# Performance work log

Hardware: AMD Instinct MI355X
Metric: run time of the kernel (lower is better)

The kernel has to match this reference:

```python
import jax, jax.numpy as jnp
import numpy as np

V, H, B, T, L, G = 32000, 256, 16, 128, 50, 8
BETA, GAMMA = 5.0, 2.0
ATOL = 1e-8  # torch.allclose(x, zeros) default atol (rtol term vanishes vs zero)


def setup_inputs() -> dict:
    key = jax.random.key(0)
    ks = jax.random.split(key, 17)
    u = 1.0 / np.sqrt(H)
    def U(k, shape):
        return jax.random.uniform(k, shape, jnp.float32, -u, u)
    return dict(
        recipe=jax.random.randint(ks[0], (B, T), 0, V),
        g=jax.random.randint(ks[1], (B, G), 0, V),
        ingr=jax.random.randint(ks[2], (B, L), 0, V),
        wv=jax.random.normal(ks[3], (V, H), jnp.float32) * 0.1,  # frozen word vectors
        w_ih=U(ks[4], (5 * H, H)),
        w_hh=U(ks[5], (5 * H, H)),
        b_ih=U(ks[6], (5 * H,)),
        b_hh=U(ks[7], (5 * H,)),
        Z=U(ks[8], (H, H)),
        Y=U(ks[9], (H, H)),
        U_g=U(ks[10], (H, H)),
        z_bias=U(ks[11], (H,)),
        y_bias=U(ks[12], (H,)),
        S=U(ks[13], (3, H)),
        P=U(ks[14], (H, H)),
        fcW=U(ks[15], (V, H)),
        fcb=U(ks[16], (V,)),
    )


def _cgru_forward(x, g_vec, E, w_ih, w_hh, b_ih, b_hh, Z, Y, U_g, z_bias, y_bias, S, P):
    # x: (B,T,H) batch_first; g_vec: (B,H); E: (B,L,H)
    ht0 = g_vec @ U_g.T                      # init_hidden
    a0 = jnp.zeros((x.shape[0], E.shape[1]), x.dtype)
    E0 = E                                   # (1-a)*E with a=0
    ot0 = jnp.zeros_like(x[:, 0])
    goal_term = g_vec @ Y.T + y_bias         # constant across steps

    def step(carry, x_t):
        ht, ot, a, E_new = carry
        is_zero = jnp.all(jnp.abs(x_t) <= ATOL)
        # --- cell ---
        gi = x_t @ w_ih.T + b_ih
        gh = ht @ w_hh.T + b_hh
        i_r, i_u, i_n, i_g, i_i = jnp.split(gi, 5, axis=1)
        h_r, h_u, h_n, h_g, h_i = jnp.split(gh, 5, axis=1)
        z_t = jax.nn.sigmoid(i_u + h_u)
        r_t = jax.nn.sigmoid(i_r + h_r)
        s_t = jax.nn.sigmoid(i_g + h_g)
        q_t = jax.nn.sigmoid(i_i + h_i)
        tmp = E_new.sum(axis=1)              # 'mlk -> mk'
        h_tilde = jnp.tanh(i_n + r_t * h_n + s_t * goal_term + q_t * (tmp @ Z.T + z_bias))
        ht2 = h_tilde + z_t * (ht - h_tilde)
        # --- attention read/write ---
        ref = jax.nn.softmax((BETA * ht2) @ S.T, axis=-1)   # (B,3)
        h_proj = ht2 @ P.T
        En = (1.0 - a)[:, :, None] * E
        alpha_n = jax.nn.softmax(GAMMA * jnp.einsum('mk,mlk->ml', h_proj, En), axis=-1)
        c_n = jnp.einsum('mlk,ml->mk', E, alpha_n)
        Eu = a[:, :, None] * E
        alpha_u = jax.nn.softmax(GAMMA * jnp.einsum('mk,mlk->ml', h_proj, Eu), axis=-1)
        c_u = jnp.einsum('mlk,ml->mk', E, alpha_u)
        out = ref[:, 0:1] * h_proj + ref[:, 1:2] * c_n + ref[:, 2:3] * c_u
        a2 = a + ref[:, 1:2] * alpha_n
        # skip update when input step is all-zero (faithful to torch.allclose guard)
        ht_o = jnp.where(is_zero, ht, ht2)
        ot_o = jnp.where(is_zero, ot, out)
        a_o = jnp.where(is_zero, a, a2)
        E_o = jnp.where(is_zero, E_new, En)
        return (ht_o, ot_o, a_o, E_o), ot_o

    (ht, ot, a, E_new), outs = jax.lax.scan(step, (ht0, ot0, a0, E0),
                                            jnp.transpose(x, (1, 0, 2)))
    output = jnp.transpose(outs, (1, 0, 2))  # back to batch_first (B,T,H)
    return output, ht, a, E_new


def reference(recipe, g, ingr, wv, w_ih, w_hh, b_ih, b_hh, Z, Y, U_g,
              z_bias, y_bias, S, P, fcW, fcb):
    recipe_embed = wv[recipe]           # (B,T,H)
    goal_embed = wv[g].sum(axis=1)      # (B,H)
    E = wv[ingr]                        # (B,L,H)
    output, ht, a, E_new = _cgru_forward(recipe_embed, goal_embed, E,
                                         w_ih, w_hh, b_ih, b_hh, Z, Y, U_g,
                                         z_bias, y_bias, S, P)
    logits = output @ fcW.T + fcb       # (B,T,V)
    return logits, ht, a, E_new
```

## Files before the change

### kernel.cpp

```cpp
#include <hip/hip_runtime.h>

#define Hd   256
#define Bd   16
#define Td   128
#define Ld   50
#define Vd   32000
#define G5H  1280

typedef __attribute__((ext_vector_type(8))) short short8v;
typedef __attribute__((ext_vector_type(4))) float f32x4;

__device__ __forceinline__ unsigned short f2bu(float f) {
  unsigned u = __float_as_uint(f);
  unsigned r = (u + 0x7fffu + ((u >> 16) & 1u)) >> 16;
  return (unsigned short)r;
}
__device__ __forceinline__ float bu2f(unsigned short b) {
  return __uint_as_float(((unsigned)b) << 16);
}
__device__ __forceinline__ float sigm(float x) { return 1.f / (1.f + __expf(-x)); }

__device__ __forceinline__ void st_devu(unsigned* p, unsigned v) {
  __hip_atomic_store(p, v, __ATOMIC_RELAXED, __HIP_MEMORY_SCOPE_AGENT);
}
__device__ __forceinline__ unsigned ld_devu(const unsigned* p) {
  return __hip_atomic_load((unsigned*)p, __ATOMIC_RELAXED, __HIP_MEMORY_SCOPE_AGENT);
}
__device__ __forceinline__ void st_devd(double* p, double v) {
  __hip_atomic_store(p, v, __ATOMIC_RELAXED, __HIP_MEMORY_SCOPE_AGENT);
}
__device__ __forceinline__ double ld_devd(const double* p) {
  return __hip_atomic_load((double*)p, __ATOMIC_RELAXED, __HIP_MEMORY_SCOPE_AGENT);
}
__device__ __forceinline__ double pk2(float a, float b) {
  union { double d; float2 f; } u; u.f = make_float2(a, b); return u.d;
}

__global__ __launch_bounds__(256) void conv_kernel(
    const float* __restrict__ wv, const float* __restrict__ w_ih,
    const float* __restrict__ fcW, const float* __restrict__ w_hh,
    const float* __restrict__ Zm, const float* __restrict__ Pm,
    unsigned short* __restrict__ wv_b, unsigned short* __restrict__ wih_b,
    unsigned short* __restrict__ fcw_b, unsigned short* __restrict__ whh_f,
    unsigned short* __restrict__ z_f, unsigned short* __restrict__ p_f)
{
  const long N0 = 2048000, N1 = N0 + 81920, N2 = N1 + 2048000;
  const long NW = 81920, NZ = 16384, NP = 16384;
  const long N5 = N2 + NW + NZ + NP;
  for (long idx = (long)blockIdx.x * blockDim.x + threadIdx.x; idx < N5;
       idx += (long)gridDim.x * blockDim.x) {
    if (idx < N2) {
      const float* src; unsigned short* dst; long off;
      if      (idx < N0) { src = wv;   dst = wv_b;  off = idx; }
      else if (idx < N1) { src = w_ih; dst = wih_b; off = idx - N0; }
      else               { src = fcW;  dst = fcw_b; off = idx - N1; }
      float4 v = *(const float4*)(src + off * 4);
      ushort4 o;
      o.x = f2bu(v.x); o.y = f2bu(v.y); o.z = f2bu(v.z); o.w = f2bu(v.w);
      *(ushort4*)(dst + off * 4) = o;
    } else {
      long u = idx - N2;
      const float* src; unsigned short* dst;
      if      (u < NW)      { src = w_hh; dst = whh_f; }
      else if (u < NW + NZ) { src = Zm;   dst = z_f;  u -= NW; }
      else                  { src = Pm;   dst = p_f;  u -= NW + NZ; }
      long frag = u >> 7;
      int g128 = (int)(u & 127);
      int lane = g128 >> 1, e0 = (g128 & 1) * 4;
      long T = frag >> 3; int ks = (int)(frag & 7);
      int lr = lane & 15, lg = lane >> 4;
      float4 v = *(const float4*)(src + (T * 16 + lr) * 256 + ks * 32 + lg * 8 + e0);
      ushort4 o;
      o.x = f2bu(v.x); o.y = f2bu(v.y); o.z = f2bu(v.z); o.w = f2bu(v.w);
      *(ushort4*)(dst + u * 4) = o;
    }
  }
}

__global__ __launch_bounds__(256) void prep_kernel(
    const int* __restrict__ g, const int* __restrict__ ingr,
    const float* __restrict__ wv, const float* __restrict__ Ug,
    const float* __restrict__ Ym, const float* __restrict__ yb,
    float* __restrict__ E_ws, float* __restrict__ sumE,
    float* __restrict__ goal_ws, float* __restrict__ HT0)
{
  __shared__ float ge[256];
  const int b = blockIdx.x, tid = threadIdx.x;
  float s = 0.f;
  for (int i = 0; i < 8; ++i) s += wv[((size_t)g[(b << 3) + i] << 8) + tid];
  ge[tid] = s;
  __syncthreads();
  float h0 = 0.f, gt = 0.f;
  const float* ur = Ug + (tid << 8);
  const float* yr = Ym + (tid << 8);
#pragma unroll 8
  for (int k = 0; k < Hd; k += 4) {
    float4 gv = *(const float4*)(ge + k);
    float4 uv = *(const float4*)(ur + k);
    float4 yv = *(const float4*)(yr + k);
    h0 = fmaf(gv.x, uv.x, h0); h0 = fmaf(gv.y, uv.y, h0);
    h0 = fmaf(gv.z, uv.z, h0); h0 = fmaf(gv.w, uv.w, h0);
    gt = fmaf(gv.x, yv.x, gt); gt = fmaf(gv.y, yv.y, gt);
    gt = fmaf(gv.z, yv.z, gt); gt = fmaf(gv.w, yv.w, gt);
  }
  HT0[(b << 8) + tid] = h0;
  goal_ws[(b << 8) + tid] = gt + yb[tid];
  float se = 0.f;
  for (int l = 0; l < Ld; ++l) {
    float v = wv[((size_t)ingr[b * Ld + l] << 8) + tid];
    E_ws[((size_t)(b * Ld + l) << 8) + tid] = v;
    se += v;
  }
  sumE[(b << 8) + tid] = se;
}

template <int MODE>
__global__ __launch_bounds__(256) void gemm_bf16(
    const unsigned short* __restrict__ A, const unsigned short* __restrict__ Bmat,
    const int* __restrict__ ridx, const float* __restrict__ bias,
    float* __restrict__ C)
{
  __shared__ unsigned short As[128 * 64];
  __shared__ unsigned short Bs[128 * 64];
  const int tid = threadIdx.x;
  const int m0 = blockIdx.x << 7, n0 = blockIdx.y << 7;
  const int wave = tid >> 6, lane = tid & 63;
  const int wm = wave >> 1, wn = wave & 1;
  const int lr = lane & 15, lg = lane >> 4;

  f32x4 acc[4][4];
#pragma unroll
  for (int i = 0; i < 4; ++i)
#pragma unroll
    for (int jj = 0; jj < 4; ++jj) acc[i][jj] = (f32x4){0.f, 0.f, 0.f, 0.f};

  const int srow = tid >> 1, shalf = tid & 1;
  const unsigned short* arow;
  {
    int gm = m0 + srow;
    if (MODE == 0) {
      int tt = gm >> 4, bb = gm & 15;
      arow = A + (size_t)ridx[bb * Td + tt] * Hd;
    } else {
      arow = A + (size_t)gm * Hd;
    }
  }
  const unsigned short* brow = Bmat + (size_t)(n0 + srow) * Hd;

  for (int k0 = 0; k0 < Hd; k0 += 64) {
#pragma unroll
    for (int c = 0; c < 4; ++c) {
      int k = shalf * 32 + c * 8;
      uint4 va = *(const uint4*)(arow + k0 + k);
      uint4 vb = *(const uint4*)(brow + k0 + k);
      int byo = (srow << 7) + ((k << 1) ^ ((srow & 7) << 4));
      *(uint4*)((char*)As + byo) = va;
      *(uint4*)((char*)Bs + byo) = vb;
    }
    __syncthreads();
#pragma unroll
    for (int kk = 0; kk < 2; ++kk) {
      short8v af[4], bfr[4];
      const int kb = kk * 32 + lg * 8;
#pragma unroll
      for (int i = 0; i < 4; ++i) {
        int ar = wm * 64 + i * 16 + lr;
        af[i] = *(const short8v*)((const char*)As + (ar << 7) + ((kb << 1) ^ ((ar & 7) << 4)));
        int br = wn * 64 + i * 16 + lr;
        bfr[i] = *(const short8v*)((const char*)Bs + (br << 7) + ((kb << 1) ^ ((br & 7) << 4)));
      }
#pragma unroll
      for (int i = 0; i < 4; ++i)
#pragma unroll
        for (int jj = 0; jj < 4; ++jj)
          acc[i][jj] = __builtin_amdgcn_mfma_f32_16x16x32_bf16(af[i], bfr[jj], acc[i][jj], 0, 0, 0);
    }
    __syncthreads();
  }
#pragma unroll
  for (int i = 0; i < 4; ++i)
#pragma unroll
    for (int jj = 0; jj < 4; ++jj) {
      int col = n0 + wn * 64 + jj * 16 + lr;
      float bv = bias[col];
#pragma unroll
      for (int r = 0; r < 4; ++r) {
        int row = m0 + wm * 64 + i * 16 + lg * 4 + r;
        float v = acc[i][jj][r] + bv;
        if (MODE == 0) {
          int tt = row >> 4, bb = row & 15;
          C[((size_t)(bb * Td + tt)) * G5H + col] = v;
        } else {
          C[(size_t)row * Vd + col] = v;
        }
      }
    }
}

#define RNN_SMEM 150080
__global__ __launch_bounds__(512, 1) void rnn_kernel(
    const unsigned short* __restrict__ whh_f, const unsigned short* __restrict__ z_f,
    const unsigned short* __restrict__ p_f, const float* __restrict__ b_hh,
    const float* __restrict__ Sm, const float* __restrict__ z_bias,
    const float* __restrict__ gi, const float* __restrict__ goal_ws,
    const float* __restrict__ E_ws, const float* __restrict__ sumE,
    const float* __restrict__ HT0,
    unsigned short* __restrict__ out_all, float* __restrict__ d_out,
    double* __restrict__ XH, double* __restrict__ XP, unsigned* __restrict__ FL)
{
  extern __shared__ char smem[];
  unsigned short* w_lds = (unsigned short*)(smem);
  unsigned short* z_lds = (unsigned short*)(smem + 81920);
  unsigned short* p_lds = (unsigned short*)(smem + 98304);
  unsigned short* E_lds = (unsigned short*)(smem + 114688);
  float* hp    = (float*)(smem + 141088);
  float* gh_l  = (float*)(smem + 142112);
  float* zd    = (float*)(smem + 142752);
  float* se    = (float*)(smem + 142880);
  float* gl    = (float*)(smem + 143904);
  float* bh    = (float*)(smem + 144032);
  float* zb    = (float*)(smem + 144672);
  float* Sl    = (float*)(smem + 144800);
  float* a_l   = (float*)(smem + 145184);
  float* d_l   = (float*)(smem + 145440);
  float* an_l  = (float*)(smem + 145696);
  float* au_l  = (float*)(smem + 145952);
  float* sd    = (float*)(smem + 146208);
  float* refl  = (float*)(smem + 146224);
  unsigned short* tp_hi = (unsigned short*)(smem + 146240);
  unsigned short* tp_lo = (unsigned short*)(smem + 146752);
  unsigned short* hs_hi = (unsigned short*)(smem + 147264);
  unsigned short* hs_lo = (unsigned short*)(smem + 147328);
  float* hrow  = (float*)(smem + 147392);
  unsigned short* ht_hi = (unsigned short*)(smem + 148416);
  unsigned short* ht_lo = (unsigned short*)(smem + 148928);
  float* gi_l  = (float*)(smem + 149440);

  const int b  = blockIdx.x >> 3;
  const int j  = blockIdx.x & 7;
  const int hc0 = j << 5;
  const int tid = threadIdx.x;
  const int lane = tid & 63, wid = tid >> 6;
  const int lr = lane & 15, lg = lane >> 4;
  unsigned* FLb = FL + (b << 5);

  for (int idx = tid; idx < 5120; idx += 512) {
    int f = idx >> 6, e = idx & 63;
    int q = f >> 3, ks = f & 7;
    int T = (q >> 1) * 16 + 2 * j + (q & 1);
    *(uint4*)(w_lds + ((size_t)f << 9) + e * 8) =
        *(const uint4*)(whh_f + (((size_t)T * 8 + ks) << 9) + e * 8);
  }
  for (int idx = tid; idx < 1024; idx += 512) {
    int f = idx >> 6, e = idx & 63;
    int T = 2 * j + (f >> 3), ks = f & 7;
    *(uint4*)(z_lds + ((size_t)f << 9) + e * 8) =
        *(const uint4*)(z_f + (((size_t)T * 8 + ks) << 9) + e * 8);
  }
  for (int idx = tid; idx < 1024; idx += 512) {
    int f = idx >> 6, e = idx & 63;
    *(uint4*)(p_lds + ((size_t)f << 9) + e * 8) =
        *(const uint4*)(p_f + (((size_t)f * 8 + j) << 9) + e * 8);
  }
  for (int idx = tid; idx < Ld * 256; idx += 512) {
    int l = idx >> 8, k = idx & 255;
    E_lds[l * 264 + (k >> 5) * 33 + (k & 31)] =
        f2bu(E_ws[((size_t)(b * Ld + l) << 8) + k]);
  }
  if (tid < 160) bh[tid] = b_hh[((tid >> 5) << 8) + hc0 + (tid & 31)];
  if (tid < 96) Sl[tid] = Sm[((tid >> 5) << 8) + hc0 + (tid & 31)];
  if (tid < 32) {
    gl[tid] = goal_ws[(b << 8) + hc0 + tid];
    zb[tid] = z_bias[hc0 + tid];
  }
  if (tid < 256) {
    float s0 = sumE[(b << 8) + tid];
    se[tid] = s0;
    unsigned short hi = f2bu(s0);
    tp_hi[tid] = hi; tp_lo[tid] = f2bu(s0 - bu2f(hi));
    float h0 = HT0[(b << 8) + tid];
    hrow[tid] = h0;
    unsigned short hh = f2bu(h0);
    ht_hi[tid] = hh; ht_lo[tid] = f2bu(h0 - bu2f(hh));
  }
  if (tid < 64) a_l[tid] = 0.f;
  __syncthreads();

  if (wid < 4) {
#pragma unroll
    for (int i = 0; i < 3; ++i) {
      int q = wid + 4 * i;
      if (q < 10) {
        f32x4 acc = (f32x4){0.f, 0.f, 0.f, 0.f};
#pragma unroll
        for (int ks = 0; ks < 8; ++ks) {
          short8v av = *(const short8v*)(w_lds + ((size_t)(q * 8 + ks) << 9) + (lane << 3));
          short8v bv = (short8v){0,0,0,0,0,0,0,0};
          if (lr < 2)
            bv = *(const short8v*)((lr == 0 ? ht_hi : ht_lo) + ks * 32 + (lg << 3));
          acc = __builtin_amdgcn_mfma_f32_16x16x32_bf16(av, bv, acc, 0, 0, 0);
        }
#pragma unroll
        for (int r = 0; r < 4; ++r) {
          float v = acc[r] + __shfl_xor(acc[r], 1);
          if (lr == 0) gh_l[q * 16 + lg * 4 + r] = v;
        }
      }
    }
  } else if (wid == 4 || wid == 5) {
    int tz = wid - 4;
    f32x4 acc = (f32x4){0.f, 0.f, 0.f, 0.f};
#pragma unroll
    for (int ks = 0; ks < 8; ++ks) {
      short8v av = *(const short8v*)(z_lds + ((size_t)(tz * 8 + ks) << 9) + (lane << 3));
      short8v bv = (short8v){0,0,0,0,0,0,0,0};
      if (lr < 2)
        bv = *(const short8v*)((lr == 0 ? tp_hi : tp_lo) + ks * 32 + (lg << 3));
      acc = __builtin_amdgcn_mfma_f32_16x16x32_bf16(av, bv, acc, 0, 0, 0);
    }
#pragma unroll
    for (int r = 0; r < 4; ++r) {
      float v = acc[r] + __shfl_xor(acc[r], 1);
      if (lr == 0) zd[tz * 16 + lg * 4 + r] = v;
    }
  }
  __syncthreads();
  {
    double* XHp = XH + ((size_t)((0 * 16 + b) * 8 + j)) * 16;
    double* XPp = XP + ((size_t)((0 * 16 + b) * 8 + j)) * 132;
    if (tid < 32) {
      int cl = tid;
      const float* gib = gi + ((size_t)(b * Td)) * G5H + hc0 + cl;
      float g_ir = gib[0], g_iu = gib[256], g_in = gib[512];
      float g_ig = gib[768], g_ii = gib[1024];
      float hr = gh_l[cl]       + bh[cl];
      float hu = gh_l[32 + cl]  + bh[32 + cl];
      float hn = gh_l[64 + cl]  + bh[64 + cl];
      float hg = gh_l[96 + cl]  + bh[96 + cl];
      float hq = gh_l[128 + cl] + bh[128 + cl];
      float rt = sigm(g_ir + hr), zt = sigm(g_iu + hu);
      float st = sigm(g_ig + hg), qt = sigm(g_ii + hq);
      float htl = tanhf(g_in + rt * hn + st * gl[cl] + qt * (zd[cl] + zb[cl]));
      float h2 = htl + zt * (hrow[hc0 + cl] - htl);
      unsigned short hi = f2bu(h2);
      hs_hi[cl] = hi; hs_lo[cl] = f2bu(h2 - bu2f(hi));
      float h2o = __shfl_xor(h2, 1);
      if (!(cl & 1)) st_devd(XHp + (cl >> 1), pk2(h2, h2o));
      float p0 = Sl[cl] * h2, p1 = Sl[32 + cl] * h2, p2 = Sl[64 + cl] * h2;
      p0 += __shfl_xor(p0, 1);  p0 += __shfl_xor(p0, 2);  p0 += __shfl_xor(p0, 4);
      p0 += __shfl_xor(p0, 8);  p0 += __shfl_xor(p0, 16);
      p1 += __shfl_xor(p1, 1);  p1 += __shfl_xor(p1, 2);  p1 += __shfl_xor(p1, 4);
      p1 += __shfl_xor(p1, 8);  p1 += __shfl_xor(p1, 16);
      p2 += __shfl_xor(p2, 1);  p2 += __shfl_xor(p2, 2);  p2 += __shfl_xor(p2, 4);
      p2 += __shfl_xor(p2, 8);  p2 += __shfl_xor(p2, 16);
      if (cl == 0) {
        st_devd(XPp + 128, pk2(p0, p1));
        st_devd(XPp + 129, pk2(p2, 0.f));
      }
    }
    __syncthreads();
#pragma unroll
    for (int qq = 0; qq < 2; ++qq) {
      int q = wid * 2 + qq;
      short8v av = *(const short8v*)(p_lds + ((size_t)q << 9) + (lane << 3));
      short8v bv = (short8v){0,0,0,0,0,0,0,0};
      if (lr < 2)
        bv = *(const short8v*)((lr == 0 ? hs_hi : hs_lo) + (lg << 3));
      f32x4 acc = (f32x4){0.f, 0.f, 0.f, 0.f};
      acc = __builtin_amdgcn_mfma_f32_16x16x32_bf16(av, bv, acc, 0, 0, 0);
      float v0 = acc[0] + __shfl_xor(acc[0], 1);
      float v1 = acc[1] + __shfl_xor(acc[1], 1);
      float v2 = acc[2] + __shfl_xor(acc[2], 1);
      float v3 = acc[3] + __shfl_xor(acc[3], 1);
      if (lr == 0) {
        st_devd(XPp + q * 8 + lg * 2, pk2(v0, v1));
        st_devd(XPp + q * 8 + lg * 2 + 1, pk2(v2, v3));
      }
    }
    asm volatile("s_waitcnt vmcnt(0)" ::: "memory");
    __syncthreads();
    if (tid == 0) st_devu(FLb + j, 1u);
  }

  for (int t = 0; t < Td; ++t) {
    const int par = t & 1, par1 = (t + 1) & 1;
    const double* XPr = XP + ((size_t)((par * 16 + b) * 8)) * 132;
    const double* XHr = XH + ((size_t)((par * 16 + b) * 8)) * 16;
    double* XPp = XP + ((size_t)((par1 * 16 + b) * 8 + j)) * 132;
    double* XHp = XH + ((size_t)((par1 * 16 + b) * 8 + j)) * 16;
    if (tid < 64) {
      unsigned tgt = (unsigned)(t + 1);
      int guard = 0;
      while (1) {
        unsigned v = (lane < 8) ? ld_devu(FLb + lane) : tgt;
        if (__all((int)(v >= tgt))) break;
        __builtin_amdgcn_s_sleep(1);
        if (++guard > (1 << 20)) break;
      }
    }
    __syncthreads();
    if (tid < 128) {
      float2 f0, f1, f2, f3, f4, f5, f6, f7;
      { union { double d; float2 f; } u_;
        u_.d = ld_devd(XPr + 0 * 132 + tid); f0 = u_.f;
        u_.d = ld_devd(XPr + 1 * 132 + tid); f1 = u_.f;
        u_.d = ld_devd(XPr + 2 * 132 + tid); f2 = u_.f;
        u_.d = ld_devd(XPr + 3 * 132 + tid); f3 = u_.f;
        u_.d = ld_devd(XPr + 4 * 132 + tid); f4 = u_.f;
        u_.d = ld_devd(XPr + 5 * 132 + tid); f5 = u_.f;
        u_.d = ld_devd(XPr + 6 * 132 + tid); f6 = u_.f;
        u_.d = ld_devd(XPr + 7 * 132 + tid); f7 = u_.f; }
      hp[2 * tid] =
        ((((((f0.x + f1.x) + f2.x) + f3.x) + f4.x) + f5.x) + f6.x) + f7.x;
      hp[2 * tid + 1] =
        ((((((f0.y + f1.y) + f2.y) + f3.y) + f4.y) + f5.y) + f6.y) + f7.y;
    } else if (tid == 128 || tid == 129) {
      int w = tid - 128;
      float2 f[8];
#pragma unroll
      for (int js = 0; js < 8; ++js) {
        union { double d; float2 f; } u_;
        u_.d = ld_devd(XPr + js * 132 + 128 + w);
        f[js] = u_.f;
      }
      float sx = ((((((f[0].x + f[1].x) + f[2].x) + f[3].x) + f[4].x) + f[5].x)
                  + f[6].x) + f[7].x;
      float sy = ((((((f[0].y + f[1].y) + f[2].y) + f[3].y) + f[4].y) + f[5].y)
                  + f[6].y) + f[7].y;
      if (w == 0) { sd[0] = sx; sd[1] = sy; }
      else        { sd[2] = sx; }
    } else if (tid >= 256 && tid < 384) {
      int u = tid - 256;
      union { double d; float2 f; } u_;
      u_.d = ld_devd(XHr + (u >> 4) * 16 + (u & 15));
      int c0 = (u >> 4) * 32 + 2 * (u & 15);
      float a0 = u_.f.x, a1 = u_.f.y;
      hrow[c0] = a0; hrow[c0 + 1] = a1;
      unsigned short h0 = f2bu(a0), h1 = f2bu(a1);
      ht_hi[c0] = h0;     ht_lo[c0] = f2bu(a0 - bu2f(h0));
      ht_hi[c0 + 1] = h1; ht_lo[c0 + 1] = f2bu(a1 - bu2f(h1));
      if (t == Td - 1 && j == 0) {
        d_out[(size_t)65536000 + (b << 8) + c0] = a0;
        d_out[(size_t)65536000 + (b << 8) + c0 + 1] = a1;
      }
    } else if (tid >= 384 && tid < 416 && t < Td - 1) {
      int u2 = tid - 384;
      const float* gib = gi + ((size_t)(b * Td + t + 1)) * G5H + hc0 + u2;
      gi_l[u2]       = gib[0];
      gi_l[32 + u2]  = gib[256];
      gi_l[64 + u2]  = gib[512];
      gi_l[96 + u2]  = gib[768];
      gi_l[128 + u2] = gib[1024];
    }
    __syncthreads();
    if (wid < 4) {
#pragma unroll
      for (int i = 0; i < 3; ++i) {
        int q = wid + 4 * i;
        if (q < 10) {
          f32x4 acc = (f32x4){0.f, 0.f, 0.f, 0.f};
#pragma unroll
          for (int ks = 0; ks < 8; ++ks) {
            short8v av = *(const short8v*)(w_lds + ((size_t)(q * 8 + ks) << 9) + (lane << 3));
            short8v bv = (short8v){0,0,0,0,0,0,0,0};
            if (lr < 2)
              bv = *(const short8v*)((lr == 0 ? ht_hi : ht_lo) + ks * 32 + (lg << 3));
            acc = __builtin_amdgcn_mfma_f32_16x16x32_bf16(av, bv, acc, 0, 0, 0);
          }
#pragma unroll
          for (int r = 0; r < 4; ++r) {
            float v = acc[r] + __shfl_xor(acc[r], 1);
            if (lr == 0) gh_l[q * 16 + lg * 4 + r] = v;
          }
        }
      }
    } else if (tid >= 256) {
      int u = tid - 256;
      if (u < 200) {
        int l = u >> 2, q = u & 3;
        const unsigned short* er0 = E_lds + l * 264 + q * 66;
        const float* hq = hp + (q << 6);
        float p = 0.f;
#pragma unroll 8
        for (int i = 0; i < 16; ++i) {
          unsigned uu = *(const unsigned*)(er0 + 2 * i);
          float e0 = __uint_as_float(uu << 16);
          float e1 = __uint_as_float(uu & 0xffff0000u);
          p = fmaf(e0, hq[2 * i], p);
          p = fmaf(e1, hq[2 * i + 1], p);
        }
        const unsigned short* er1 = er0 + 33;
        const float* hq1 = hq + 32;
#pragma unroll 8
        for (int i = 0; i < 16; ++i) {
          unsigned uu = *(const unsigned*)(er1 + 2 * i);
          float e0 = __uint_as_float(uu << 16);
          float e1 = __uint_as_float(uu & 0xffff0000u);
          p = fmaf(e0, hq1[2 * i], p);
          p = fmaf(e1, hq1[2 * i + 1], p);
        }
        p += __shfl_xor(p, 1); p += __shfl_xor(p, 2);
        if (q == 0) d_l[l] = p;
      } else if (u == 224) {
        float s0 = 5.0f * sd[0], s1 = 5.0f * sd[1], s2 = 5.0f * sd[2];
        float m = fmaxf(s0, fmaxf(s1, s2));
        float e0 = __expf(s0 - m), e1 = __expf(s1 - m), e2 = __expf(s2 - m);
        float inv = 1.f / (e0 + e1 + e2);
        refl[0] = e0 * inv; refl[1] = e1 * inv; refl[2] = e2 * inv;
      }
    }
    __syncthreads();
    if (tid >= 256 && tid < 384) {
      int u = tid - 256;
      int which = u >> 6;
      int l = u & 63;
      float dv;
      if (which == 0) dv = (l < Ld) ? 2.0f * (1.f - a_l[l]) * d_l[l] : -3.4e38f;
      else            dv = (l < Ld) ? 2.0f * a_l[l] * d_l[l]         : -3.4e38f;
      float m = dv;
      m = fmaxf(m, __shfl_xor(m, 1));  m = fmaxf(m, __shfl_xor(m, 2));
      m = fmaxf(m, __shfl_xor(m, 4));  m = fmaxf(m, __shfl_xor(m, 8));
      m = fmaxf(m, __shfl_xor(m, 16)); m = fmaxf(m, __shfl_xor(m, 32));
      float e = (l < Ld) ? __expf(dv - m) : 0.f;
      float ss = e;
      ss += __shfl_xor(ss, 1);  ss += __shfl_xor(ss, 2);  ss += __shfl_xor(ss, 4);
      ss += __shfl_xor(ss, 8);  ss += __shfl_xor(ss, 16); ss += __shfl_xor(ss, 32);
      float al = e / ss;
      if (which == 0) an_l[l] = al; else au_l[l] = al;
    }
    __syncthreads();
    if (tid >= 256) {
      int k = tid - 256;
      int kp = (k >> 5) * 33 + (k & 31);
      float accn = 0.f, accu = 0.f, acct = 0.f;
#pragma unroll 10
      for (int l = 0; l < Ld; ++l) {
        float e = bu2f(E_lds[l * 264 + kp]);
        accn = fmaf(an_l[l], e, accn);
        accu = fmaf(au_l[l], e, accu);
        acct = fmaf(a_l[l], e, acct);
      }
      float outv = refl[0] * hp[k] + refl[1] * accn + refl[2] * accu;
      float tn = se[k] - acct;
      unsigned short th = f2bu(tn);
      tp_hi[k] = th; tp_lo[k] = f2bu(tn - bu2f(th));
      if ((t & 7) == j) {
        out_all[(((b << 7) + t) << 8) + k] = f2bu(outv);
        if (t == Td - 1) {
          for (int l = 0; l < Ld; ++l) {
            size_t o = ((size_t)(b * Ld + l) << 8) + k;
            d_out[(size_t)65540896 + o] = (1.f - a_l[l]) * E_ws[o];
          }
        }
      }
    }
    __syncthreads();
    if (tid < 128) {
      int tz = wid;
      f32x4 acc = (f32x4){0.f, 0.f, 0.f, 0.f};
#pragma unroll
      for (int ks = 0; ks < 8; ++ks) {
        short8v av = *(const short8v*)(z_lds + ((size_t)(tz * 8 + ks) << 9) + (lane << 3));
        short8v bv = (short8v){0,0,0,0,0,0,0,0};
        if (lr < 2)
          bv = *(const short8v*)((lr == 0 ? tp_hi : tp_lo) + ks * 32 + (lg << 3));
        acc = __builtin_amdgcn_mfma_f32_16x16x32_bf16(av, bv, acc, 0, 0, 0);
      }
#pragma unroll
      for (int r = 0; r < 4; ++r) {
        float v = acc[r] + __shfl_xor(acc[r], 1);
        if (lr == 0) zd[tz * 16 + lg * 4 + r] = v;
      }
    } else if (tid >= 256 && tid < 256 + Ld) {
      int l = tid - 256;
      float na = a_l[l] + refl[1] * an_l[l];
      a_l[l] = na;
      if (t == Td - 1 && j == 7) d_out[(size_t)65540096 + b * Ld + l] = na;
    }
    __syncthreads();
    if (t < Td - 1 && tid < 32) {
      int cl = tid;
      float hr = gh_l[cl]       + bh[cl];
      float hu = gh_l[32 + cl]  + bh[32 + cl];
      float hn = gh_l[64 + cl]  + bh[64 + cl];
      float hg = gh_l[96 + cl]  + bh[96 + cl];
      float hq = gh_l[128 + cl] + bh[128 + cl];
      float rt = sigm(gi_l[cl] + hr), zt = sigm(gi_l[32 + cl] + hu);
      float st = sigm(gi_l[96 + cl] + hg), qt = sigm(gi_l[128 + cl] + hq);
      float htl = tanhf(gi_l[64 + cl] + rt * hn + st * gl[cl] + qt * (zd[cl] + zb[cl]));
      float h2 = htl + zt * (hrow[hc0 + cl] - htl);
      unsigned short hi = f2bu(h2);
      hs_hi[cl] = hi; hs_lo[cl] = f2bu(h2 - bu2f(hi));
      float h2o = __shfl_xor(h2, 1);
      if (!(cl & 1)) st_devd(XHp + (cl >> 1), pk2(h2, h2o));
      float p0 = Sl[cl] * h2, p1 = Sl[32 + cl] * h2, p2 = Sl[64 + cl] * h2;
      p0 += __shfl_xor(p0, 1);  p0 += __shfl_xor(p0, 2);  p0 += __shfl_xor(p0, 4);
      p0 += __shfl_xor(p0, 8);  p0 += __shfl_xor(p0, 16);
      p1 += __shfl_xor(p1, 1);  p1 += __shfl_xor(p1, 2);  p1 += __shfl_xor(p1, 4);
      p1 += __shfl_xor(p1, 8);  p1 += __shfl_xor(p1, 16);
      p2 += __shfl_xor(p2, 1);  p2 += __shfl_xor(p2, 2);  p2 += __shfl_xor(p2, 4);
      p2 += __shfl_xor(p2, 8);  p2 += __shfl_xor(p2, 16);
      if (cl == 0) {
        st_devd(XPp + 128, pk2(p0, p1));
        st_devd(XPp + 129, pk2(p2, 0.f));
      }
    }
    __syncthreads();
    if (t < Td - 1) {
#pragma unroll
      for (int qq = 0; qq < 2; ++qq) {
        int q = wid * 2 + qq;
        short8v av = *(const short8v*)(p_lds + ((size_t)q << 9) + (lane << 3));
        short8v bv = (short8v){0,0,0,0,0,0,0,0};
        if (lr < 2)
          bv = *(const short8v*)((lr == 0 ? hs_hi : hs_lo) + (lg << 3));
        f32x4 acc = (f32x4){0.f, 0.f, 0.f, 0.f};
        acc = __builtin_amdgcn_mfma_f32_16x16x32_bf16(av, bv, acc, 0, 0, 0);
        float v0 = acc[0] + __shfl_xor(acc[0], 1);
        float v1 = acc[1] + __shfl_xor(acc[1], 1);
        float v2 = acc[2] + __shfl_xor(acc[2], 1);
        float v3 = acc[3] + __shfl_xor(acc[3], 1);
        if (lr == 0) {
          st_devd(XPp + q * 8 + lg * 2, pk2(v0, v1));
          st_devd(XPp + q * 8 + lg * 2 + 1, pk2(v2, v3));
        }
      }
    }
    asm volatile("s_waitcnt vmcnt(0)" ::: "memory");
    __syncthreads();
    if (t < Td - 1 && tid == 0) st_devu(FLb + j, (unsigned)(t + 2));
  }
}

extern "C" void kernel_launch(void* const* d_in, const int* in_sizes, int n_in,
                              void* d_out, int out_size, void* d_ws, size_t ws_size,
                              hipStream_t stream)
{
  const int*   recipe = (const int*)d_in[0];
  const int*   g      = (const int*)d_in[1];
  const int*   ingr   = (const int*)d_in[2];
  const float* wv     = (const float*)d_in[3];
  const float* w_ih   = (const float*)d_in[4];
  const float* w_hh   = (const float*)d_in[5];
  const float* b_ih   = (const float*)d_in[6];
  const float* b_hh   = (const float*)d_in[7];
  const float* Z      = (const float*)d_in[8];
  const float* Y      = (const float*)d_in[9];
  const float* Ug     = (const float*)d_in[10];
  const float* z_bias = (const float*)d_in[11];
  const float* y_bias = (const float*)d_in[12];
  const float* S      = (const float*)d_in[13];
  const float* P      = (const float*)d_in[14];
  const float* fcW    = (const float*)d_in[15];
  const float* fcb    = (const float*)d_in[16];
  float* out = (float*)d_out;
  char* ws = (char*)d_ws;

  size_t off = 0;
  unsigned* FL             = (unsigned*)(ws + off);        off += 2048;
  double* XH               = (double*)(ws + off);          off += 32768;
  double* XP               = (double*)(ws + off);          off += 270336;
  unsigned short* wv_b     = (unsigned short*)(ws + off);  off += 16384000;
  unsigned short* wih_b    = (unsigned short*)(ws + off);  off += 655360;
  unsigned short* fcw_b    = (unsigned short*)(ws + off);  off += 16384000;
  unsigned short* whh_f    = (unsigned short*)(ws + off);  off += 655360;
  unsigned short* z_f      = (unsigned short*)(ws + off);  off += 131072;
  unsigned short* p_f      = (unsigned short*)(ws + off);  off += 131072;
  float* gi_ws             = (float*)(ws + off);           off += 10485760;
  float* E_ws              = (float*)(ws + off);           off += 819200;
  float* sumE              = (float*)(ws + off);           off += 16384;
  float* goal_ws           = (float*)(ws + off);           off += 16384;
  float* HT0               = (float*)(ws + off);           off += 16384;
  unsigned short* out_all  = (unsigned short*)(ws + off);  off += 1048576;

  hipMemsetAsync(FL, 0, 2048, stream);
  conv_kernel<<<4096, 256, 0, stream>>>(wv, w_ih, fcW, w_hh, Z, P,
                                        wv_b, wih_b, fcw_b, whh_f, z_f, p_f);
  prep_kernel<<<16, 256, 0, stream>>>(g, ingr, wv, Ug, Y, y_bias,
                                      E_ws, sumE, goal_ws, HT0);
  gemm_bf16<0><<<dim3(16, 10), 256, 0, stream>>>(wv_b, wih_b, recipe, b_ih, gi_ws);
  hipFuncSetAttribute((const void*)rnn_kernel,
                      hipFuncAttributeMaxDynamicSharedMemorySize, RNN_SMEM);
  rnn_kernel<<<128, 512, RNN_SMEM, stream>>>(whh_f, z_f, p_f, b_hh, S, z_bias,
                                             gi_ws, goal_ws, E_ws, sumE, HT0,
                                             out_all, out, XH, XP, FL);
  gemm_bf16<1><<<dim3(16, 250), 256, 0, stream>>>(out_all, fcw_b, nullptr, fcb, out);
}
```

Measured before the change: 1.530 ms.

## Reschedule recurrent step to overlap off-critical work with inter-block wait

Reorders the per-timestep phases of the persistent recurrent kernel. Computing the a-weighted E sum for the Z-projection input moves into the first phase, where it runs alongside the spin-wait on other blocks' flags. The Z matmul now runs in parallel with the w_hh matmul, and the GRU cell update runs alongside the attention softmax. This removes about two block barriers per step and shortens the critical path between publishing partial results and the next step. The cost is more complex warp-role assignment and ordering hazards around a_l, whose update is moved after the output computation.

After: 1.405 ms. 8.2% less time.

```diff
diff --git a/kernel.cpp b/kernel.cpp
--- a/kernel.cpp
+++ b/kernel.cpp
@@ -388,7 +388,17 @@
     const double* XHr = XH + ((size_t)((par * 16 + b) * 8)) * 16;
     double* XPp = XP + ((size_t)((par1 * 16 + b) * 8 + j)) * 132;
     double* XHp = XH + ((size_t)((par1 * 16 + b) * 8 + j)) * 16;
-    if (tid < 64) {
+    if (tid < 256) {
+      int k = tid;
+      int kp = (k >> 5) * 33 + (k & 31);
+      float acct = 0.f;
+#pragma unroll 10
+      for (int l = 0; l < Ld; ++l)
+        acct = fmaf(a_l[l], bu2f(E_lds[l * 264 + kp]), acct);
+      float tn = se[k] - acct;
+      unsigned short th = f2bu(tn);
+      tp_hi[k] = th; tp_lo[k] = f2bu(tn - bu2f(th));
+    } else {
       unsigned tgt = (unsigned)(t + 1);
       int guard = 0;
       while (1) {
@@ -397,84 +407,106 @@
         __builtin_amdgcn_s_sleep(1);
         if (++guard > (1 << 20)) break;
       }
+      int u = tid - 256;
+      if (u < 128) {
+        float2 f0, f1, f2, f3, f4, f5, f6, f7;
+        { union { double d; float2 f; } u_;
+          u_.d = ld_devd(XPr + 0 * 132 + u); f0 = u_.f;
+          u_.d = ld_devd(XPr + 1 * 132 + u); f1 = u_.f;
+          u_.d = ld_devd(XPr + 2 * 132 + u); f2 = u_.f;
+          u_.d = ld_devd(XPr + 3 * 132 + u); f3 = u_.f;
+          u_.d = ld_devd(XPr + 4 * 132 + u); f4 = u_.f;
+          u_.d = ld_devd(XPr + 5 * 132 + u); f5 = u_.f;
+          u_.d = ld_devd(XPr + 6 * 132 + u); f6 = u_.f;
+          u_.d = ld_devd(XPr + 7 * 132 + u); f7 = u_.f; }
+        hp[2 * u] =
+          ((((((f0.x + f1.x) + f2.x) + f3.x) + f4.x) + f5.x) + f6.x) + f7.x;
+        hp[2 * u + 1] =
+          ((((((f0.y + f1.y) + f2.y) + f3.y) + f4.y) + f5.y) + f6.y) + f7.y;
+      } else if (u < 192) {
+        int d0 = 2 * (u - 128);
+#pragma unroll
+        for (int s = 0; s < 2; ++s) {
+          int d = d0 + s;
+          union { double d; float2 f; } u_;
+          u_.d = ld_devd(XHr + (d >> 4) * 16 + (d & 15));
+          int c0 = (d >> 4) * 32 + 2 * (d & 15);
+          float a0 = u_.f.x, a1 = u_.f.y;
+          hrow[c0] = a0; hrow[c0 + 1] = a1;
+          unsigned short h0 = f2bu(a0), h1 = f2bu(a1);
+          ht_hi[c0] = h0;     ht_lo[c0] = f2bu(a0 - bu2f(h0));
+          ht_hi[c0 + 1] = h1; ht_lo[c0 + 1] = f2bu(a1 - bu2f(h1));
+          if (t == Td - 1 && j == 0) {
+            d_out[(size_t)65536000 + (b << 8) + c0] = a0;
+            d_out[(size_t)65536000 + (b << 8) + c0 + 1] = a1;
+          }
+        }
+      } else {
+        int u2 = u - 192;
+        if (u2 < 3) {
+          float2 f[8];
+#pragma unroll
+          for (int js = 0; js < 8; ++js) {
+            union { double d; float2 f; } u_;
+            u_.d = ld_devd(XPr + js * 132 + 128 + (u2 >> 1));
+            f[js] = u_.f;
+          }
+          float sx, sy;
+          sx = ((((((f[0].x + f[1].x) + f[2].x) + f[3].x) + f[4].x) + f[5].x)
+                + f[6].x) + f[7].x;
+          sy = ((((((f[0].y + f[1].y) + f[2].y) + f[3].y) + f[4].y) + f[5].y)
+                + f[6].y) + f[7].y;
+          sd[u2] = (u2 & 1) ? sy : ((u2 == 0) ? sx : sx);
+          if (u2 == 0) { sd[0] = sx; sd[1] = sy; }
+          else if (u2 == 2) sd[2] = sx;
+        } else if (u2 >= 8 && u2 < 40 && t < Td - 1) {
+          int c = u2 - 8;
+          const float* gib = gi + ((size_t)(b * Td + t + 1)) * G5H + hc0 + c;
+          gi_l[c]       = gib[0];
+          gi_l[32 + c]  = gib[256];
+          gi_l[64 + c]  = gib[512];
+          gi_l[96 + c]  = gib[768];
+          gi_l[128 + c] = gib[1024];
+        }
+      }
     }
     __syncthreads();
-    if (tid < 128) {
-      float2 f0, f1, f2, f3, f4, f5, f6, f7;
-      { union { double d; float2 f; } u_;
-        u_.d = ld_devd(XPr + 0 * 132 + tid); f0 = u_.f;
-        u_.d = ld_devd(XPr + 1 * 132 + tid); f1 = u_.f;
-        u_.d = ld_devd(XPr + 2 * 132 + tid); f2 = u_.f;
-        u_.d = ld_devd(XPr + 3 * 132 + tid); f3 = u_.f;
-        u_.d = ld_devd(XPr + 4 * 132 + tid); f4 = u_.f;
-        u_.d = ld_devd(XPr + 5 * 132 + tid); f5 = u_.f;
-        u_.d = ld_devd(XPr + 6 * 132 + tid); f6 = u_.f;
-        u_.d = ld_devd(XPr + 7 * 132 + tid); f7 = u_.f; }
-      hp[2 * tid] =
-        ((((((f0.x + f1.x) + f2.x) + f3.x) + f4.x) + f5.x) + f6.x) + f7.x;
-      hp[2 * tid + 1] =
-        ((((((f0.y + f1.y) + f2.y) + f3.y) + f4.y) + f5.y) + f6.y) + f7.y;
-    } else if (tid == 128 || tid == 129) {
-      int w = tid - 128;
-      float2 f[8];
-#pragma unroll
-      for (int js = 0; js < 8; ++js) {
-        union { double d; float2 f; } u_;
-        u_.d = ld_devd(XPr + js * 132 + 128 + w);
-        f[js] = u_.f;
-      }
-      float sx = ((((((f[0].x + f[1].x) + f[2].x) + f[3].x) + f[4].x) + f[5].x)
-                  + f[6].x) + f[7].x;
-      float sy = ((((((f[0].y + f[1].y) + f[2].y) + f[3].y) + f[4].y) + f[5].y)
-                  + f[6].y) + f[7].y;
-      if (w == 0) { sd[0] = sx; sd[1] = sy; }
-      else        { sd[2] = sx; }
-    } else if (tid >= 256 && tid < 384) {
-      int u = tid - 256;
-      union { double d; float2 f; } u_;
-      u_.d = ld_devd(XHr + (u >> 4) * 16 + (u & 15));
-      int c0 = (u >> 4) * 32 + 2 * (u & 15);
-      float a0 = u_.f.x, a1 = u_.f.y;
-      hrow[c0] = a0; hrow[c0 + 1] = a1;
-      unsigned short h0 = f2bu(a0), h1 = f2bu(a1);
-      ht_hi[c0] = h0;     ht_lo[c0] = f2bu(a0 - bu2f(h0));
-      ht_hi[c0 + 1] = h1; ht_lo[c0 + 1] = f2bu(a1 - bu2f(h1));
-      if (t == Td - 1 && j == 0) {
-        d_out[(size_t)65536000 + (b << 8) + c0] = a0;
-        d_out[(size_t)65536000 + (b << 8) + c0 + 1] = a1;
-      }
-    } else if (tid >= 384 && tid < 416 && t < Td - 1) {
-      int u2 = tid - 384;
-      const float* gib = gi + ((size_t)(b * Td + t + 1)) * G5H + hc0 + u2;
-      gi_l[u2]       = gib[0];
-      gi_l[32 + u2]  = gib[256];
-      gi_l[64 + u2]  = gib[512];
-      gi_l[96 + u2]  = gib[768];
-      gi_l[128 + u2] = gib[1024];
-    }
-    __syncthreads();
-    if (wid < 4) {
-#pragma unroll
-      for (int i = 0; i < 3; ++i) {
-        int q = wid + 4 * i;
-        if (q < 10) {
-          f32x4 acc = (f32x4){0.f, 0.f, 0.f, 0.f};
-#pragma unroll
-          for (int ks = 0; ks < 8; ++ks) {
-            short8v av = *(const short8v*)(w_lds + ((size_t)(q * 8 + ks) << 9) + (lane << 3));
-            short8v bv = (short8v){0,0,0,0,0,0,0,0};
-            if (lr < 2)
-              bv = *(const short8v*)((lr == 0 ? ht_hi : ht_lo) + ks * 32 + (lg << 3));
-            acc = __builtin_amdgcn_mfma_f32_16x16x32_bf16(av, bv, acc, 0, 0, 0);
-          }
-#pragma unroll
-          for (int r = 0; r < 4; ++r) {
-            float v = acc[r] + __shfl_xor(acc[r], 1);
-            if (lr == 0) gh_l[q * 16 + lg * 4 + r] = v;
-          }
-        }
-      }
-    } else if (tid >= 256) {
+    if (wid < 2) {
+      int tz = wid;
+      f32x4 acc = (f32x4){0.f, 0.f, 0.f, 0.f};
+#pragma unroll
+      for (int ks = 0; ks < 8; ++ks) {
+        short8v av = *(const short8v*)(z_lds + ((size_t)(tz * 8 + ks) << 9) + (lane << 3));
+        short8v bv = (short8v){0,0,0,0,0,0,0,0};
+        if (lr < 2)
+          bv = *(const short8v*)((lr == 0 ? tp_hi : tp_lo) + ks * 32 + (lg << 3));
+        acc = __builtin_amdgcn_mfma_f32_16x16x32_bf16(av, bv, acc, 0, 0, 0);
+      }
+#pragma unroll
+      for (int r = 0; r < 4; ++r) {
+        float v = acc[r] + __shfl_xor(acc[r], 1);
+        if (lr == 0) zd[tz * 16 + lg * 4 + r] = v;
+      }
+    } else if (wid < 4) {
+#pragma unroll
+      for (int i = 0; i < 5; ++i) {
+        int q = (wid - 2) * 5 + i;
+        f32x4 acc = (f32x4){0.f, 0.f, 0.f, 0.f};
+#pragma unroll
+        for (int ks = 0; ks < 8; ++ks) {
+          short8v av = *(const short8v*)(w_lds + ((size_t)(q * 8 + ks) << 9) + (lane << 3));
+          short8v bv = (short8v){0,0,0,0,0,0,0,0};
+          if (lr < 2)
+            bv = *(const short8v*)((lr == 0 ? ht_hi : ht_lo) + ks * 32 + (lg << 3));
+          acc = __builtin_amdgcn_mfma_f32_16x16x32_bf16(av, bv, acc, 0, 0, 0);
+        }
+#pragma unroll
+        for (int r = 0; r < 4; ++r) {
+          float v = acc[r] + __shfl_xor(acc[r], 1);
+          if (lr == 0) gh_l[q * 16 + lg * 4 + r] = v;
+        }
+      }
+    } else {
       int u = tid - 256;
       if (u < 200) {
         int l = u >> 2, q = u & 3;
@@ -501,7 +533,7 @@
         }
         p += __shfl_xor(p, 1); p += __shfl_xor(p, 2);
         if (q == 0) d_l[l] = p;
-      } else if (u == 224) {
+      } else if (u == 204) {
         float s0 = 5.0f * sd[0], s1 = 5.0f * sd[1], s2 = 5.0f * sd[2];
         float m = fmaxf(s0, fmaxf(s1, s2));
         float e0 = __expf(s0 - m), e1 = __expf(s1 - m), e2 = __expf(s2 - m);
@@ -510,8 +542,36 @@
       }
     }
     __syncthreads();
-    if (tid >= 256 && tid < 384) {
-      int u = tid - 256;
+    if (tid < 32) {
+      if (t < Td - 1) {
+        int cl = tid;
+        float hr = gh_l[cl]       + bh[cl];
+        float hu = gh_l[32 + cl]  + bh[32 + cl];
+        float hn = gh_l[64 + cl]  + bh[64 + cl];
+        float hg = gh_l[96 + cl]  + bh[96 + cl];
+        float hq = gh_l[128 + cl] + bh[128 + cl];
+        float rt = sigm(gi_l[cl] + hr), zt = sigm(gi_l[32 + cl] + hu);
+        float st = sigm(gi_l[96 + cl] + hg), qt = sigm(gi_l[128 + cl] + hq);
+        float htl = tanhf(gi_l[64 + cl] + rt * hn + st * gl[cl] + qt * (zd[cl] + zb[cl]));
+        float h2 = htl + zt * (hrow[hc0 + cl] - htl);
+        unsigned short hi = f2bu(h2);
+        hs_hi[cl] = hi; hs_lo[cl] = f2bu(h2 - bu2f(hi));
+        float h2o = __shfl_xor(h2, 1);
+        if (!(cl & 1)) st_devd(XHp + (cl >> 1), pk2(h2, h2o));
+        float p0 = Sl[cl] * h2, p1 = Sl[32 + cl] * h2, p2 = Sl[64 + cl] * h2;
+        p0 += __shfl_xor(p0, 1);  p0 += __shfl_xor(p0, 2);  p0 += __shfl_xor(p0, 4);
+        p0 += __shfl_xor(p0, 8);  p0 += __shfl_xor(p0, 16);
+        p1 += __shfl_xor(p1, 1);  p1 += __shfl_xor(p1, 2);  p1 += __shfl_xor(p1, 4);
+        p1 += __shfl_xor(p1, 8);  p1 += __shfl_xor(p1, 16);
+        p2 += __shfl_xor(p2, 1);  p2 += __shfl_xor(p2, 2);  p2 += __shfl_xor(p2, 4);
+        p2 += __shfl_xor(p2, 8);  p2 += __shfl_xor(p2, 16);
+        if (cl == 0) {
+          st_devd(XPp + 128, pk2(p0, p1));
+          st_devd(XPp + 129, pk2(p2, 0.f));
+        }
+      }
+    } else if (tid >= 64 && tid < 192) {
+      int u = tid - 64;
       int which = u >> 6;
       int l = u & 63;
       float dv;
@@ -529,21 +589,38 @@
       if (which == 0) an_l[l] = al; else au_l[l] = al;
     }
     __syncthreads();
-    if (tid >= 256) {
+    if (wid < 4) {
+      if (t < Td - 1) {
+#pragma unroll
+        for (int qq = 0; qq < 4; ++qq) {
+          int q = wid * 4 + qq;
+          short8v av = *(const short8v*)(p_lds + ((size_t)q << 9) + (lane << 3));
+          short8v bv = (short8v){0,0,0,0,0,0,0,0};
+          if (lr < 2)
+            bv = *(const short8v*)((lr == 0 ? hs_hi : hs_lo) + (lg << 3));
+          f32x4 acc = (f32x4){0.f, 0.f, 0.f, 0.f};
+          acc = __builtin_amdgcn_mfma_f32_16x16x32_bf16(av, bv, acc, 0, 0, 0);
+          float v0 = acc[0] + __shfl_xor(acc[0], 1);
+          float v1 = acc[1] + __shfl_xor(acc[1], 1);
+          float v2 = acc[2] + __shfl_xor(acc[2], 1);
+          float v3 = acc[3] + __shfl_xor(acc[3], 1);
+          if (lr == 0) {
+            st_devd(XPp + q * 8 + lg * 2, pk2(v0, v1));
+            st_devd(XPp + q * 8 + lg * 2 + 1, pk2(v2, v3));
+          }
+        }
+      }
+    } else {
       int k = tid - 256;
       int kp = (k >> 5) * 33 + (k & 31);
-      float accn = 0.f, accu = 0.f, acct = 0.f;
+      float accn = 0.f, accu = 0.f;
 #pragma unroll 10
       for (int l = 0; l < Ld; ++l) {
         float e = bu2f(E_lds[l * 264 + kp]);
         accn = fmaf(an_l[l], e, accn);
         accu = fmaf(au_l[l], e, accu);
-        acct = fmaf(a_l[l], e, acct);
       }
       float outv = refl[0] * hp[k] + refl[1] * accn + refl[2] * accu;
-      float tn = se[k] - acct;
-      unsigned short th = f2bu(tn);
-      tp_hi[k] = th; tp_lo[k] = f2bu(tn - bu2f(th));
       if ((t & 7) == j) {
         out_all[(((b << 7) + t) << 8) + k] = f2bu(outv);
         if (t == Td - 1) {
@@ -553,82 +630,19 @@
           }
         }
       }
-    }
-    __syncthreads();
-    if (tid < 128) {
-      int tz = wid;
-      f32x4 acc = (f32x4){0.f, 0.f, 0.f, 0.f};
-#pragma unroll
-      for (int ks = 0; ks < 8; ++ks) {
-        short8v av = *(const short8v*)(z_lds + ((size_t)(tz * 8 + ks) << 9) + (lane << 3));
-        short8v bv = (short8v){0,0,0,0,0,0,0,0};
-        if (lr < 2)
-          bv = *(const short8v*)((lr == 0 ? tp_hi : tp_lo) + ks * 32 + (lg << 3));
-        acc = __builtin_amdgcn_mfma_f32_16x16x32_bf16(av, bv, acc, 0, 0, 0);
-      }
-#pragma unroll
-      for (int r = 0; r < 4; ++r) {
-        float v = acc[r] + __shfl_xor(acc[r], 1);
-        if (lr == 0) zd[tz * 16 + lg * 4 + r] = v;
-      }
-    } else if (tid >= 256 && tid < 256 + Ld) {
-      int l = tid - 256;
-      float na = a_l[l] + refl[1] * an_l[l];
-      a_l[l] = na;
-      if (t == Td - 1 && j == 7) d_out[(size_t)65540096 + b * Ld + l] = na;
-    }
-    __syncthreads();
-    if (t < Td - 1 && tid < 32) {
-      int cl = tid;
-      float hr = gh_l[cl]       + bh[cl];
-      float hu = gh_l[32 + cl]  + bh[32 + cl];
-      float hn = gh_l[64 + cl]  + bh[64 + cl];
-      float hg = gh_l[96 + cl]  + bh[96 + cl];
-      float hq = gh_l[128 + cl] + bh[128 + cl];
-      float rt = sigm(gi_l[cl] + hr), zt = sigm(gi_l[32 + cl] + hu);
-      float st = sigm(gi_l[96 + cl] + hg), qt = sigm(gi_l[128 + cl] + hq);
-      float htl = tanhf(gi_l[64 + cl] + rt * hn + st * gl[cl] + qt * (zd[cl] + zb[cl]));
-      float h2 = htl + zt * (hrow[hc0 + cl] - htl);
-      unsigned short hi = f2bu(h2);
-      hs_hi[cl] = hi; hs_lo[cl] = f2bu(h2 - bu2f(hi));
-      float h2o = __shfl_xor(h2, 1);
-      if (!(cl & 1)) st_devd(XHp + (cl >> 1), pk2(h2, h2o));
-      float p0 = Sl[cl] * h2, p1 = Sl[32 + cl] * h2, p2 = Sl[64 + cl] * h2;
-      p0 += __shfl_xor(p0, 1);  p0 += __shfl_xor(p0, 2);  p0 += __shfl_xor(p0, 4);
-      p0 += __shfl_xor(p0, 8);  p0 += __shfl_xor(p0, 16);
-      p1 += __shfl_xor(p1, 1);  p1 += __shfl_xor(p1, 2);  p1 += __shfl_xor(p1, 4);
-      p1 += __shfl_xor(p1, 8);  p1 += __shfl_xor(p1, 16);
-      p2 += __shfl_xor(p2, 1);  p2 += __shfl_xor(p2, 2);  p2 += __shfl_xor(p2, 4);
-      p2 += __shfl_xor(p2, 8);  p2 += __shfl_xor(p2, 16);
-      if (cl == 0) {
-        st_devd(XPp + 128, pk2(p0, p1));
-        st_devd(XPp + 129, pk2(p2, 0.f));
-      }
-    }
+      if (t < Td - 1 && k < Ld)
+        a_l[k] = a_l[k] + refl[1] * an_l[k];
+    }
+    asm volatile("s_waitcnt vmcnt(0)" ::: "memory");
     __syncthreads();
     if (t < Td - 1) {
-#pragma unroll
-      for (int qq = 0; qq < 2; ++qq) {
-        int q = wid * 2 + qq;
-        short8v av = *(const short8v*)(p_lds + ((size_t)q << 9) + (lane << 3));
-        short8v bv = (short8v){0,0,0,0,0,0,0,0};
-        if (lr < 2)
-          bv = *(const short8v*)((lr == 0 ? hs_hi : hs_lo) + (lg << 3));
-        f32x4 acc = (f32x4){0.f, 0.f, 0.f, 0.f};
-        acc = __builtin_amdgcn_mfma_f32_16x16x32_bf16(av, bv, acc, 0, 0, 0);
-        float v0 = acc[0] + __shfl_xor(acc[0], 1);
-        float v1 = acc[1] + __shfl_xor(acc[1], 1);
-        float v2 = acc[2] + __shfl_xor(acc[2], 1);
-        float v3 = acc[3] + __shfl_xor(acc[3], 1);
-        if (lr == 0) {
-          st_devd(XPp + q * 8 + lg * 2, pk2(v0, v1));
-          st_devd(XPp + q * 8 + lg * 2 + 1, pk2(v2, v3));
-        }
-      }
-    }
-    asm volatile("s_waitcnt vmcnt(0)" ::: "memory");
-    __syncthreads();
-    if (t < Td - 1 && tid == 0) st_devu(FLb + j, (unsigned)(t + 2));
+      if (tid == 0) st_devu(FLb + j, (unsigned)(t + 2));
+    } else {
+      if (tid < Ld) {
+        float na = a_l[tid] + refl[1] * an_l[tid];
+        if (j == 7) d_out[(size_t)65540096 + b * Ld + tid] = na;
+      }
+    }
   }
 }
 
```
